# Kernel optimization log

Measured on AMD Instinct MI355X. Metric: run time of the kernel, lower is better.

## Reference

```python
import jax, jax.numpy as jnp
import numpy as np

NUM_EXPERTS = 16
HIDDEN = 2048
INTERMEDIATE = 1408
TOTAL_TOKENS = 32768  # tokens pre-sorted by expert assignment


def setup_inputs() -> dict:
    key = jax.random.key(0)
    k1, k2, k3, k4 = jax.random.split(key, 4)
    x = jax.random.normal(k1, (TOTAL_TOKENS, HIDDEN), dtype=jnp.float32)
    # normal() initializer per module; scale ~N(0, 0.02) like typical kernel_init
    w_gate = jax.random.normal(k2, (NUM_EXPERTS, HIDDEN, INTERMEDIATE), dtype=jnp.float32) * 0.02
    w_up = jax.random.normal(k3, (NUM_EXPERTS, HIDDEN, INTERMEDIATE), dtype=jnp.float32) * 0.02
    w_down = jax.random.normal(k4, (NUM_EXPERTS, INTERMEDIATE, HIDDEN), dtype=jnp.float32) * 0.02
    # tokens evenly distributed over experts; sums to TOTAL_TOKENS
    group_sizes = jnp.full((NUM_EXPERTS,), TOTAL_TOKENS // NUM_EXPERTS, dtype=jnp.int32)
    return {"x": x, "w_gate": w_gate, "w_up": w_up, "w_down": w_down,
            "group_sizes": group_sizes}


def reference(x, w_gate, w_up, w_down, group_sizes):
    # Grouped (ragged) GEMMs: rows of x are grouped contiguously by expert,
    # group_sizes[e] rows use expert e's kernel. lax.ragged_dot is the
    # idiomatic grouped-GEMM primitive (no dense [T,E] masking).
    gate = jax.lax.ragged_dot(x, w_gate, group_sizes)      # [T, I]
    up = jax.lax.ragged_dot(x, w_up, group_sizes)          # [T, I]
    h = jax.nn.silu(gate) * up                             # fused SwiGLU gating
    out = jax.lax.ragged_dot(h, w_down, group_sizes)       # [T, H]
    return out
```

## Files before the change

### kernel.cpp

```cpp
#include <hip/hip_runtime.h>
#include <hip/hip_bf16.h>

#define TOKENS 32768
#define NEXP   16
#define HID    2048
#define IMD    1408
#define BM 256
#define BK 64

typedef __bf16 bf16x8 __attribute__((ext_vector_type(8)));
typedef float  f32x4  __attribute__((ext_vector_type(4)));
typedef unsigned short u16x8 __attribute__((ext_vector_type(8)));

using gptr1_t = const __attribute__((address_space(1))) void*;
using lptr3_t = __attribute__((address_space(3))) void*;

static __device__ __forceinline__ unsigned short f2bf(float f) {
  unsigned int x = __builtin_bit_cast(unsigned int, f);
  x += 0x7fffu + ((x >> 16) & 1u);
  return (unsigned short)(x >> 16);
}
static __device__ __forceinline__ float bf2f(unsigned short u) {
  unsigned int x = ((unsigned int)u) << 16;
  return __builtin_bit_cast(float, x);
}
static __device__ __forceinline__ void gload16(const void* g, void* l) {
  __builtin_amdgcn_global_load_lds((gptr1_t)g, (lptr3_t)l, 16, 0, 0);
}
static __device__ __forceinline__ void vwait(int n) {
  switch (n) {
    case 0:  asm volatile("s_waitcnt vmcnt(0)" ::: "memory"); break;
    case 2:  asm volatile("s_waitcnt vmcnt(2)" ::: "memory"); break;
    default: asm volatile("s_waitcnt vmcnt(6)" ::: "memory"); break;
  }
}

__global__ __launch_bounds__(256)
void convert_kernel(const float* __restrict__ in, unsigned short* __restrict__ out, size_t n)
{
  size_t i = ((size_t)blockIdx.x * blockDim.x + threadIdx.x) * 8;
  if (i >= n) return;
  float4 a = *(const float4*)(in + i);
  float4 b = *(const float4*)(in + i + 4);
  u16x8 o;
  o[0] = f2bf(a.x); o[1] = f2bf(a.y); o[2] = f2bf(a.z); o[3] = f2bf(a.w);
  o[4] = f2bf(b.x); o[5] = f2bf(b.y); o[6] = f2bf(b.z); o[7] = f2bf(b.w);
  *(u16x8*)(out + i) = o;
}

__global__ __launch_bounds__(256)
void transpose_conv_kernel(const float* __restrict__ in, unsigned short* __restrict__ out,
                           int K, int N)
{
  __shared__ float tile[32][33];
  const int e = blockIdx.z;
  const float* ip = in + (size_t)e * K * N;
  unsigned short* op = out + (size_t)e * K * N;
  const int c0 = blockIdx.x * 32, r0 = blockIdx.y * 32;
  const int tx = threadIdx.x, ty = threadIdx.y;
#pragma unroll
  for (int i = 0; i < 4; ++i)
    tile[ty + 8 * i][tx] = ip[(size_t)(r0 + ty + 8 * i) * N + c0 + tx];
  __syncthreads();
#pragma unroll
  for (int i = 0; i < 4; ++i)
    op[(size_t)(c0 + ty + 8 * i) * K + r0 + tx] = f2bf(tile[tx][ty + 8 * i]);
}

template<int MODE>
__global__ __launch_bounds__(512, 2)
void gemm_kernel(const unsigned short* __restrict__ A,
                 const unsigned short* __restrict__ B0,
                 const unsigned short* __restrict__ B1,
                 unsigned short* __restrict__ Hc,
                 float* __restrict__ Cf,
                 const int* __restrict__ gs,
                 int K, int N)
{
  constexpr int NRT = TOKENS / BM;

  __shared__ __align__(16) unsigned short lA[2][256 * 64];
  __shared__ __align__(16) unsigned short lB[2][256 * 64];

  const int nwg = gridDim.x;
  const int q = nwg >> 3;
  const int wgid = (blockIdx.x & 7) * q + (blockIdx.x >> 3);
  const int rt = wgid % NRT;
  const int ct = wgid / NRT;
  const int row0 = rt * BM;

  int e = 0;
  { int a0 = 0;
    for (int i = 0; i < NEXP; ++i) { int s = gs[i]; if (row0 < a0 + s) { e = i; break; } a0 += s; } }

  const unsigned short* Ap = A + (size_t)row0 * K;
  const unsigned short* Bg = B0 + (size_t)e * N * K;
  const unsigned short* Bu = (MODE == 0) ? (B1 + (size_t)e * N * K) : nullptr;

  const int tid  = threadIdx.x;
  const int lane = tid & 63, wave = tid >> 6;
  const int wr = wave >> 2, wc = wave & 3;
  const int fr = lane & 15, fq = lane >> 4;

  const int csw0 = ((0 * 4 + fq) ^ (fr & 7)) * 8;
  const int csw1 = ((1 * 4 + fq) ^ (fr & 7)) * 8;

  const int r8   = lane >> 3;
  const int slog = ((lane & 7) ^ (r8 & 7)) * 8;

  const int nt = K / BK;

  f32x4 acc[8][4] = {};

  auto stage = [&](int chunk, int tt) {
    const int buf = tt & 1;
    const int k0 = tt * BK;
#pragma unroll
    for (int w = 0; w < 2; ++w) {
      if (chunk >= 2) {
        const int mh = chunk - 2;
        unsigned short* ldst = &lA[buf][(mh * 128 + w * 64 + wave * 8) * 64];
        const int grow = w * 128 + mh * 64 + wave * 8 + r8;
        gload16(Ap + (size_t)grow * K + k0 + slog, ldst);
      } else {
        const int h = chunk;
        unsigned short* ldst = &lB[buf][(h * 128 + w * 64 + wave * 8) * 64];
        const int rem = w * 64 + wave * 8 + r8;
        const int wcs = rem >> 5, rr = rem & 31;
        if constexpr (MODE == 0) {
          const int gcol = ct * 128 + (wcs * 2 + h) * 16 + (rr & 15);
          const unsigned short* mb = ((rr >> 4) & 1) ? Bu : Bg;
          gload16(mb + (size_t)gcol * K + k0 + slog, ldst);
        } else {
          const int gcol = ct * 256 + wcs * 64 + h * 32 + rr;
          gload16(Bg + (size_t)gcol * K + k0 + slog, ldst);
        }
      }
    }
  };

  bf16x8 a[4], b[4];
  auto phase = [&](int cur, int mh, int kk, bool readB,
                   int stChunk, int tN, bool doStage, int waitN) {
    const unsigned short* Ab = lA[cur];
    const unsigned short* Bb = lB[cur];
    const int csw = kk ? csw1 : csw0;
#pragma unroll
    for (int mf = 0; mf < 4; ++mf)
      a[mf] = *(const bf16x8*)(Ab + (mh * 128 + wr * 64 + mf * 16 + fr) * 64 + csw);
    if (readB) {
#pragma unroll
      for (int nf = 0; nf < 4; ++nf)
        b[nf] = *(const bf16x8*)(Bb + ((nf >> 1) * 128 + wc * 32 + (nf & 1) * 16 + fr) * 64 + csw);
    }
    if (doStage) stage(stChunk, tN);
    __builtin_amdgcn_s_barrier();
    asm volatile("s_waitcnt lgkmcnt(0)" ::: "memory");
    __builtin_amdgcn_s_setprio(1);
#pragma unroll
    for (int mf = 0; mf < 4; ++mf)
#pragma unroll
      for (int nf = 0; nf < 4; ++nf)
        acc[mh * 4 + mf][nf] =
            __builtin_amdgcn_mfma_f32_16x16x32_bf16(a[mf], b[nf], acc[mh * 4 + mf][nf], 0, 0, 0);
    __builtin_amdgcn_s_setprio(0);
    if (waitN >= 0) vwait(waitN);
    __builtin_amdgcn_s_barrier();
  };

  stage(0, 0); stage(1, 0); stage(2, 0); stage(3, 0);
  vwait(0);
  __builtin_amdgcn_s_barrier();

  for (int t = 0; t < nt; ++t) {
    const int cur = t & 1;
    const bool more = (t + 1 < nt);
    phase(cur, 0, 0, true,  0, t + 1, more, more ? 2 : 0);
    phase(cur, 1, 0, false, 1, t + 1, more, -1);
    phase(cur, 0, 1, true,  2, t + 1, more, -1);
    phase(cur, 1, 1, false, 3, t + 1, more, more ? 2 : -1);
  }

#pragma unroll
  for (int mi = 0; mi < 8; ++mi) {
    const int rowb = row0 + wr * 128 + (mi >> 2) * 64 + (mi & 3) * 16 + fq * 4;
    if constexpr (MODE == 0) {
#pragma unroll
      for (int m2 = 0; m2 < 2; ++m2) {
        const int col = ct * 128 + (wc * 2 + m2) * 16 + fr;
        f32x4 g = acc[mi][2 * m2], u = acc[mi][2 * m2 + 1];
#pragma unroll
        for (int r = 0; r < 4; ++r) {
          float gv = g[r];
          float s = gv / (1.f + __expf(-gv)) * u[r];
          Hc[(size_t)(rowb + r) * N + col] = f2bf(s);
        }
      }
    } else {
#pragma unroll
      for (int nf = 0; nf < 4; ++nf) {
        const int col = ct * 256 + wc * 64 + nf * 16 + fr;
        f32x4 v = acc[mi][nf];
#pragma unroll
        for (int r = 0; r < 4; ++r)
          Cf[(size_t)(rowb + r) * N + col] = v[r];
      }
    }
  }
}

extern "C" void kernel_launch(void* const* d_in, const int* in_sizes, int n_in,
                              void* d_out, int out_size, void* d_ws, size_t ws_size,
                              hipStream_t stream)
{
  const float* x  = (const float*)d_in[0];
  const float* wg = (const float*)d_in[1];
  const float* wu = (const float*)d_in[2];
  const float* wd = (const float*)d_in[3];
  const int*   gs = (const int*)d_in[4];
  float* out = (float*)d_out;

  const size_t SZ_XB = (size_t)TOKENS * HID * 2;
  const size_t SZ_W  = (size_t)NEXP * HID * IMD * 2;
  const size_t SZ_H  = (size_t)TOKENS * IMD * 2;
  if (ws_size < SZ_XB + 2 * SZ_W + SZ_H) return;

  char* ws = (char*)d_ws;
  unsigned short* xb  = (unsigned short*)ws;
  unsigned short* wTg = (unsigned short*)(ws + SZ_XB);
  unsigned short* wTu = (unsigned short*)(ws + SZ_XB + SZ_W);
  unsigned short* h   = (unsigned short*)(ws + SZ_XB + 2 * SZ_W);

  const int cvt_grid = (int)(((size_t)TOKENS * HID) / (256 * 8));
  convert_kernel<<<cvt_grid, 256, 0, stream>>>(x, xb, (size_t)TOKENS * HID);

  transpose_conv_kernel<<<dim3(IMD / 32, HID / 32, NEXP), dim3(32, 8), 0, stream>>>(wg, wTg, HID, IMD);
  transpose_conv_kernel<<<dim3(IMD / 32, HID / 32, NEXP), dim3(32, 8), 0, stream>>>(wu, wTu, HID, IMD);
  gemm_kernel<0><<<(TOKENS / BM) * (IMD / 128), 512, 0, stream>>>(
      xb, wTg, wTu, h, nullptr, gs, HID, IMD);

  transpose_conv_kernel<<<dim3(HID / 32, IMD / 32, NEXP), dim3(32, 8), 0, stream>>>(wd, wTg, IMD, HID);
  gemm_kernel<1><<<(TOKENS / BM) * (HID / 256), 512, 0, stream>>>(
      h, wTg, nullptr, nullptr, out, gs, IMD, HID);
}
```

Measured before the change: 931.1 us.

## Shrink GEMM tile to 128x256x32 with simple double-buffered loop

```diff
diff --git a/kernel.cpp b/kernel.cpp
--- a/kernel.cpp
+++ b/kernel.cpp
@@ -5,8 +5,8 @@
 #define NEXP   16
 #define HID    2048
 #define IMD    1408
-#define BM 256
-#define BK 64
+#define BM 128
+#define BK 32
 
 typedef __bf16 bf16x8 __attribute__((ext_vector_type(8)));
 typedef float  f32x4  __attribute__((ext_vector_type(4)));
@@ -20,19 +20,8 @@
   x += 0x7fffu + ((x >> 16) & 1u);
   return (unsigned short)(x >> 16);
 }
-static __device__ __forceinline__ float bf2f(unsigned short u) {
-  unsigned int x = ((unsigned int)u) << 16;
-  return __builtin_bit_cast(float, x);
-}
 static __device__ __forceinline__ void gload16(const void* g, void* l) {
   __builtin_amdgcn_global_load_lds((gptr1_t)g, (lptr3_t)l, 16, 0, 0);
-}
-static __device__ __forceinline__ void vwait(int n) {
-  switch (n) {
-    case 0:  asm volatile("s_waitcnt vmcnt(0)" ::: "memory"); break;
-    case 2:  asm volatile("s_waitcnt vmcnt(2)" ::: "memory"); break;
-    default: asm volatile("s_waitcnt vmcnt(6)" ::: "memory"); break;
-  }
 }
 
 __global__ __launch_bounds__(256)
@@ -67,24 +56,24 @@
     op[(size_t)(c0 + ty + 8 * i) * K + r0 + tx] = f2bf(tile[tx][ty + 8 * i]);
 }
 
-template<int MODE>
-__global__ __launch_bounds__(512, 2)
+template<int MODE, int K, int N>
+__global__ __launch_bounds__(512, 4)
 void gemm_kernel(const unsigned short* __restrict__ A,
-                 const unsigned short* __restrict__ B0,
-                 const unsigned short* __restrict__ B1,
+                 const unsigned short* __restrict__ B0m,
+                 const unsigned short* __restrict__ B1m,
                  unsigned short* __restrict__ Hc,
                  float* __restrict__ Cf,
-                 const int* __restrict__ gs,
-                 int K, int N)
+                 const int* __restrict__ gs)
 {
   constexpr int NRT = TOKENS / BM;
-
-  __shared__ __align__(16) unsigned short lA[2][256 * 64];
-  __shared__ __align__(16) unsigned short lB[2][256 * 64];
+  constexpr int nt  = K / BK;
+
+  __shared__ __align__(16) unsigned short lA[2][128 * 32];
+  __shared__ __align__(16) unsigned short lB[2][256 * 32];
 
   const int nwg = gridDim.x;
-  const int q = nwg >> 3;
-  const int wgid = (blockIdx.x & 7) * q + (blockIdx.x >> 3);
+  const int qq = nwg >> 3;
+  const int wgid = (blockIdx.x & 7) * qq + (blockIdx.x >> 3);
   const int rt = wgid % NRT;
   const int ct = wgid / NRT;
   const int row0 = rt * BM;
@@ -94,113 +83,93 @@
     for (int i = 0; i < NEXP; ++i) { int s = gs[i]; if (row0 < a0 + s) { e = i; break; } a0 += s; } }
 
   const unsigned short* Ap = A + (size_t)row0 * K;
-  const unsigned short* Bg = B0 + (size_t)e * N * K;
-  const unsigned short* Bu = (MODE == 0) ? (B1 + (size_t)e * N * K) : nullptr;
+  const unsigned short* Bg = B0m + (size_t)e * N * K;
+  const unsigned short* Bu = (MODE == 0) ? (B1m + (size_t)e * N * K) : nullptr;
 
   const int tid  = threadIdx.x;
   const int lane = tid & 63, wave = tid >> 6;
   const int wr = wave >> 2, wc = wave & 3;
   const int fr = lane & 15, fq = lane >> 4;
 
-  const int csw0 = ((0 * 4 + fq) ^ (fr & 7)) * 8;
-  const int csw1 = ((1 * 4 + fq) ^ (fr & 7)) * 8;
-
-  const int r8   = lane >> 3;
-  const int slog = ((lane & 7) ^ (r8 & 7)) * 8;
-
-  const int nt = K / BK;
-
-  f32x4 acc[8][4] = {};
-
-  auto stage = [&](int chunk, int tt) {
+  const int csw = ((fq + (fr >> 1)) & 3) * 8;
+
+  const int slotLog = ((tid & 3) - ((tid >> 3) & 3)) & 3;
+  const int srcCol = slotLog * 8;
+  const int vr = tid >> 2;
+
+  const unsigned short* aSrc = Ap + (size_t)vr * K + srcCol;
+  const unsigned short* bSrc0;
+  const unsigned short* bSrc1;
+  if constexpr (MODE == 0) {
+    const int v0 = vr, v1 = 128 + vr;
+    const int p0 = (v0 >> 4) & 1, p1 = (v1 >> 4) & 1;
+    const int c0 = ct * 128 + (v0 >> 5) * 16 + (v0 & 15);
+    const int c1 = ct * 128 + (v1 >> 5) * 16 + (v1 & 15);
+    bSrc0 = (p0 ? Bu : Bg) + (size_t)c0 * K + srcCol;
+    bSrc1 = (p1 ? Bu : Bg) + (size_t)c1 * K + srcCol;
+  } else {
+    bSrc0 = Bg + (size_t)(ct * 256 + vr) * K + srcCol;
+    bSrc1 = Bg + (size_t)(ct * 256 + 128 + vr) * K + srcCol;
+  }
+
+  const int dA  = wave * 512;
+  const int dB0 = wave * 512;
+  const int dB1 = 4096 + wave * 512;
+
+  auto STAGE = [&](int tt) {
     const int buf = tt & 1;
     const int k0 = tt * BK;
-#pragma unroll
-    for (int w = 0; w < 2; ++w) {
-      if (chunk >= 2) {
-        const int mh = chunk - 2;
-        unsigned short* ldst = &lA[buf][(mh * 128 + w * 64 + wave * 8) * 64];
-        const int grow = w * 128 + mh * 64 + wave * 8 + r8;
-        gload16(Ap + (size_t)grow * K + k0 + slog, ldst);
-      } else {
-        const int h = chunk;
-        unsigned short* ldst = &lB[buf][(h * 128 + w * 64 + wave * 8) * 64];
-        const int rem = w * 64 + wave * 8 + r8;
-        const int wcs = rem >> 5, rr = rem & 31;
-        if constexpr (MODE == 0) {
-          const int gcol = ct * 128 + (wcs * 2 + h) * 16 + (rr & 15);
-          const unsigned short* mb = ((rr >> 4) & 1) ? Bu : Bg;
-          gload16(mb + (size_t)gcol * K + k0 + slog, ldst);
-        } else {
-          const int gcol = ct * 256 + wcs * 64 + h * 32 + rr;
-          gload16(Bg + (size_t)gcol * K + k0 + slog, ldst);
-        }
-      }
-    }
+    gload16(aSrc + k0, &lA[buf][dA]);
+    gload16(bSrc0 + k0, &lB[buf][dB0]);
+    gload16(bSrc1 + k0, &lB[buf][dB1]);
   };
 
-  bf16x8 a[4], b[4];
-  auto phase = [&](int cur, int mh, int kk, bool readB,
-                   int stChunk, int tN, bool doStage, int waitN) {
-    const unsigned short* Ab = lA[cur];
-    const unsigned short* Bb = lB[cur];
-    const int csw = kk ? csw1 : csw0;
-#pragma unroll
-    for (int mf = 0; mf < 4; ++mf)
-      a[mf] = *(const bf16x8*)(Ab + (mh * 128 + wr * 64 + mf * 16 + fr) * 64 + csw);
-    if (readB) {
-#pragma unroll
-      for (int nf = 0; nf < 4; ++nf)
-        b[nf] = *(const bf16x8*)(Bb + ((nf >> 1) * 128 + wc * 32 + (nf & 1) * 16 + fr) * 64 + csw);
-    }
-    if (doStage) stage(stChunk, tN);
-    __builtin_amdgcn_s_barrier();
-    asm volatile("s_waitcnt lgkmcnt(0)" ::: "memory");
-    __builtin_amdgcn_s_setprio(1);
-#pragma unroll
-    for (int mf = 0; mf < 4; ++mf)
-#pragma unroll
-      for (int nf = 0; nf < 4; ++nf)
-        acc[mh * 4 + mf][nf] =
-            __builtin_amdgcn_mfma_f32_16x16x32_bf16(a[mf], b[nf], acc[mh * 4 + mf][nf], 0, 0, 0);
-    __builtin_amdgcn_s_setprio(0);
-    if (waitN >= 0) vwait(waitN);
-    __builtin_amdgcn_s_barrier();
-  };
-
-  stage(0, 0); stage(1, 0); stage(2, 0); stage(3, 0);
-  vwait(0);
-  __builtin_amdgcn_s_barrier();
-
+  f32x4 acc[4][4] = {};
+
+  STAGE(0);
+  __syncthreads();
+
+#pragma unroll 1
   for (int t = 0; t < nt; ++t) {
-    const int cur = t & 1;
-    const bool more = (t + 1 < nt);
-    phase(cur, 0, 0, true,  0, t + 1, more, more ? 2 : 0);
-    phase(cur, 1, 0, false, 1, t + 1, more, -1);
-    phase(cur, 0, 1, true,  2, t + 1, more, -1);
-    phase(cur, 1, 1, false, 3, t + 1, more, more ? 2 : -1);
+    const int buf = t & 1;
+    if (t + 1 < nt) STAGE(t + 1);
+
+    bf16x8 a[4], b[4];
+#pragma unroll
+    for (int m = 0; m < 4; ++m)
+      a[m] = *(const bf16x8*)(&lA[buf][(wr * 64 + m * 16 + fr) * 32 + csw]);
+#pragma unroll
+    for (int n = 0; n < 4; ++n)
+      b[n] = *(const bf16x8*)(&lB[buf][(wc * 64 + n * 16 + fr) * 32 + csw]);
+
+#pragma unroll
+    for (int m = 0; m < 4; ++m)
+#pragma unroll
+      for (int n = 0; n < 4; ++n)
+        acc[m][n] = __builtin_amdgcn_mfma_f32_16x16x32_bf16(a[m], b[n], acc[m][n], 0, 0, 0);
+
+    __syncthreads();
   }
 
 #pragma unroll
-  for (int mi = 0; mi < 8; ++mi) {
-    const int rowb = row0 + wr * 128 + (mi >> 2) * 64 + (mi & 3) * 16 + fq * 4;
+  for (int mf = 0; mf < 4; ++mf) {
+    const int rowb = row0 + wr * 64 + mf * 16 + fq * 4;
     if constexpr (MODE == 0) {
 #pragma unroll
       for (int m2 = 0; m2 < 2; ++m2) {
         const int col = ct * 128 + (wc * 2 + m2) * 16 + fr;
-        f32x4 g = acc[mi][2 * m2], u = acc[mi][2 * m2 + 1];
+        f32x4 g = acc[mf][2 * m2], u = acc[mf][2 * m2 + 1];
 #pragma unroll
         for (int r = 0; r < 4; ++r) {
           float gv = g[r];
-          float s = gv / (1.f + __expf(-gv)) * u[r];
-          Hc[(size_t)(rowb + r) * N + col] = f2bf(s);
+          Hc[(size_t)(rowb + r) * N + col] = f2bf(gv / (1.f + __expf(-gv)) * u[r]);
         }
       }
     } else {
 #pragma unroll
       for (int nf = 0; nf < 4; ++nf) {
         const int col = ct * 256 + wc * 64 + nf * 16 + fr;
-        f32x4 v = acc[mi][nf];
+        f32x4 v = acc[mf][nf];
 #pragma unroll
         for (int r = 0; r < 4; ++r)
           Cf[(size_t)(rowb + r) * N + col] = v[r];
@@ -236,10 +205,10 @@
 
   transpose_conv_kernel<<<dim3(IMD / 32, HID / 32, NEXP), dim3(32, 8), 0, stream>>>(wg, wTg, HID, IMD);
   transpose_conv_kernel<<<dim3(IMD / 32, HID / 32, NEXP), dim3(32, 8), 0, stream>>>(wu, wTu, HID, IMD);
-  gemm_kernel<0><<<(TOKENS / BM) * (IMD / 128), 512, 0, stream>>>(
-      xb, wTg, wTu, h, nullptr, gs, HID, IMD);
+  gemm_kernel<0, HID, IMD><<<(TOKENS / BM) * (IMD / 128), 512, 0, stream>>>(
+      xb, wTg, wTu, h, nullptr, gs);
 
   transpose_conv_kernel<<<dim3(HID / 32, IMD / 32, NEXP), dim3(32, 8), 0, stream>>>(wd, wTg, IMD, HID);
-  gemm_kernel<1><<<(TOKENS / BM) * (HID / 256), 512, 0, stream>>>(
-      h, wTg, nullptr, nullptr, out, gs, IMD, HID);
-}
+  gemm_kernel<1, IMD, HID><<<(TOKENS / BM) * (HID / 256), 512, 0, stream>>>(
+      h, wTg, nullptr, nullptr, out, gs);
+}
```

Result: slower. 949.8 us (+2.0%).
